# Kernel tuning notes

Measured on AMD Instinct MI355X. Metric: run time of the kernel, lower is better.

The kernel has to match this reference:

```python
import jax, jax.numpy as jnp
import numpy as np

D_STATE = 512
D_MODEL = 512
BATCH = 8
SEQ = 4096
DT_MIN, DT_MAX = 1e-3, 0.1
LN_EPS = 1e-5


def setup_inputs() -> dict:
    key = jax.random.key(0)
    ks = jax.random.split(key, 4)
    x = jax.random.normal(ks[0], (BATCH, SEQ, D_MODEL), dtype=jnp.float32)
    volatility_scale = jax.random.uniform(ks[1], (BATCH, SEQ, 1), dtype=jnp.float32)
    # parameters (mirroring the torch module's __init__)
    log_lambda_real = jnp.linspace(np.log(DT_MIN), np.log(DT_MAX), D_STATE).astype(jnp.float32)
    log_b = jax.random.uniform(ks[2], (D_STATE, 1), dtype=jnp.float32, minval=-0.5, maxval=0.5)
    c = jax.random.normal(ks[3], (1, D_STATE), dtype=jnp.float32) / np.sqrt(D_STATE)
    log_d = jnp.zeros((1,), jnp.float32)
    ts = np.array([1.0 / 24.0, 1.0, 5.0, 21.0, 63.0], np.float32)
    extra = np.linspace(63.0, 189.0, D_STATE - len(ts), dtype=np.float32)
    log_step = jnp.log(jnp.asarray(np.concatenate([ts, extra])))
    volatility_gate = jnp.ones((D_MODEL,), jnp.float32)
    alpha = jnp.asarray(0.7, jnp.float32)
    ln_weight = jnp.ones((D_STATE,), jnp.float32)
    ln_bias = jnp.zeros((D_STATE,), jnp.float32)
    return dict(x=x, volatility_scale=volatility_scale,
                log_lambda_real=log_lambda_real, log_b=log_b, c=c, log_d=log_d,
                log_step=log_step, volatility_gate=volatility_gate, alpha=alpha,
                ln_weight=ln_weight, ln_bias=ln_bias)


def reference(x, volatility_scale, log_lambda_real, log_b, c, log_d,
              log_step, volatility_gate, alpha, ln_weight, ln_bias):
    lam = -jnp.exp(log_lambda_real)              # [N], negative real poles
    step = jnp.exp(log_step)                     # [N], per-state timescale
    b = jnp.exp(log_b)[:, 0]                     # [N]
    d = jnp.exp(log_d)                           # [1], skip gain
    # bilinear (Tustin) discretization, paired per state
    z = step * lam                               # [N]
    a_disc = (2.0 + z) / (2.0 - z)               # [N]
    b_disc = step * (1.0 + a_disc) * b / 2.0     # [N]
    gate = jax.nn.sigmoid(volatility_gate)       # [D]
    c_vec = c[0]                                 # [N]

    def layer_norm(h):
        mu = jnp.mean(h, axis=-1, keepdims=True)
        var = jnp.var(h, axis=-1, keepdims=True)
        return (h - mu) * jax.lax.rsqrt(var + LN_EPS) * ln_weight + ln_bias

    def scan_step(h, inp):
        x_t, v_t = inp                           # [B,D], [B,1]
        h = a_disc * h + b_disc * x_t            # diagonal SSM update, [B,N]
        h = layer_norm(h)
        h = h / (1.0 + gate * v_t)               # volatility gating
        y_t = jnp.sum(h * c_vec, axis=-1, keepdims=True) + d * x_t  # [B,D]
        return h, y_t

    h0 = jnp.zeros((x.shape[0], a_disc.shape[0]), x.dtype)
    xs = (jnp.swapaxes(x, 0, 1), jnp.swapaxes(volatility_scale, 0, 1))  # time-major
    _, ys = jax.lax.scan(scan_step, h0, xs)      # [S,B,D]
    y = jnp.swapaxes(ys, 0, 1)                   # [B,S,D]
    al = jax.nn.sigmoid(alpha)
    return al * x + (1.0 - al) * y
```

## Files before the change

### kernel.cpp

```cpp
#include <hip/hip_runtime.h>
#include <cstdint>
#include <cstddef>

#define BATCH 8
#define SEQ   4096
#define DS    512
#define JPL   8
#define BLK   4
#define NB    (SEQ / BLK)

typedef float v2f __attribute__((ext_vector_type(2)));
typedef float v4f __attribute__((ext_vector_type(4)));

static __device__ __forceinline__ v2f lo2(v4f x) { return __builtin_shufflevector(x, x, 0, 1); }
static __device__ __forceinline__ v2f hi2(v4f x) { return __builtin_shufflevector(x, x, 2, 3); }

template <int CTRL>
__device__ __forceinline__ float dpp_add(float v) {
  int t = __builtin_amdgcn_update_dpp(0, __builtin_bit_cast(int, v), CTRL, 0xF, 0xF, true);
  return v + __builtin_bit_cast(float, t);
}
__device__ __forceinline__ float wave_sum64(float v) {
  v = dpp_add<0x111>(v);
  v = dpp_add<0x112>(v);
  v = dpp_add<0x114>(v);
  v = dpp_add<0x118>(v);
  v = dpp_add<0x142>(v);
  v = dpp_add<0x143>(v);
  return v;
}
__device__ __forceinline__ float bcast63(float v) {
  return __builtin_bit_cast(float, __builtin_amdgcn_readlane(__builtin_bit_cast(int, v), 63));
}

__global__ __launch_bounds__(256) void rg_kernel(const float* __restrict__ vol,
                                                 const float* __restrict__ vgat,
                                                 float* __restrict__ rg) {
  int idx = blockIdx.x * 256 + threadIdx.x;
  int nt  = idx & 127;
  int bt  = idx >> 7;
  float v = vol[bt];
  v4f g = *(const v4f*)(vgat + nt * 4);
  v4f r;
#pragma unroll
  for (int k = 0; k < 4; ++k) {
    float gg = 1.0f / (1.0f + expf(-g[k]));
    r[k] = 1.0f / (1.0f + gg * v);
  }
  *(v4f*)(rg + (size_t)idx * 4) = r;
}

template <bool RGP, bool PART>
__global__ __launch_bounds__(64, 1) void ssm_scan(
    const float* __restrict__ x, const float* __restrict__ vol,
    const float* __restrict__ llr, const float* __restrict__ logb,
    const float* __restrict__ cvec, const float* __restrict__ lstp,
    const float* __restrict__ vgat, const float* __restrict__ lnw,
    const float* __restrict__ lnb, const float* __restrict__ rg_g,
    float* __restrict__ outp)
{
  const int b    = blockIdx.x;
  const int lane = threadIdx.x;
  const int n0   = lane * JPL;

  v2f a[4], bd[4], w[4], bias[4], cc[4], gate[4];
#pragma unroll
  for (int j = 0; j < JPL; ++j) {
    int n = n0 + j;
    float lam = -expf(llr[n]);
    float st  = expf(lstp[n]);
    float z   = st * lam;
    float ad  = (2.0f + z) / (2.0f - z);
    a[j >> 1][j & 1]    = ad;
    bd[j >> 1][j & 1]   = st * (1.0f + ad) * expf(logb[n]) * 0.5f;
    w[j >> 1][j & 1]    = lnw[n];
    bias[j >> 1][j & 1] = lnb[n];
    cc[j >> 1][j & 1]   = cvec[n];
    gate[j >> 1][j & 1] = RGP ? 0.0f : (1.0f / (1.0f + expf(-vgat[n])));
  }

  const float* xp = x + (size_t)b * SEQ * DS + n0;
  const float* vp = vol + (size_t)b * SEQ;
  const float* rp = RGP ? (rg_g + (size_t)b * SEQ * DS + n0) : nullptr;
  float* pp = outp + (size_t)b * SEQ * (PART ? 64 : 1);

  v2f h[4];
#pragma unroll
  for (int k = 0; k < 4; ++k) h[k] = (v2f){0.0f, 0.0f};

  v4f XA[2 * BLK], XB[2 * BLK], RA[2 * BLK], RB[2 * BLK];
  v4f VA = {0, 0, 0, 0}, VB = {0, 0, 0, 0};

  auto load_blk = [&](v4f (&X)[2 * BLK], v4f (&R)[2 * BLK], v4f& V, int T) {
    const float* xb = xp + (size_t)T * DS;
#pragma unroll
    for (int u = 0; u < BLK; ++u) {
      X[2 * u]     = *(const v4f*)(xb + u * DS);
      X[2 * u + 1] = *(const v4f*)(xb + u * DS + 4);
    }
    if constexpr (RGP) {
      const float* rb = rp + (size_t)T * DS;
#pragma unroll
      for (int u = 0; u < BLK; ++u) {
        R[2 * u]     = *(const v4f*)(rb + u * DS);
        R[2 * u + 1] = *(const v4f*)(rb + u * DS + 4);
      }
    } else {
      V = *(const v4f*)(vp + T);
    }
  };

  auto proc_blk = [&](const v4f (&X)[2 * BLK], const v4f (&R)[2 * BLK], v4f V, int T) {
    float sacc[BLK];
#pragma unroll
    for (int u = 0; u < BLK; ++u) {
      v2f xs[4] = {lo2(X[2 * u]), hi2(X[2 * u]), lo2(X[2 * u + 1]), hi2(X[2 * u + 1])};

      v2f hr[4];
#pragma unroll
      for (int k = 0; k < 4; ++k)
        hr[k] = __builtin_elementwise_fma(a[k], h[k], bd[k] * xs[k]);

      v2f t01 = hr[0] + hr[1], t23 = hr[2] + hr[3];
      v2f ts = t01 + t23;
      float s1 = ts.x + ts.y;
      v2f q01 = hr[0] * hr[0] + hr[1] * hr[1];
      v2f q23 = hr[2] * hr[2] + hr[3] * hr[3];
      v2f qs = q01 + q23;
      float s2 = qs.x + qs.y;

      s1 = bcast63(wave_sum64(s1));
      s2 = bcast63(wave_sum64(s2));
      float mu  = s1 * (1.0f / DS);
      float m2  = s2 * (1.0f / DS);
      float var = __builtin_fmaf(-mu, mu, m2);
      float inv = __builtin_amdgcn_rsqf(var + 1e-5f);

      v2f rs[4];
      if constexpr (RGP) {
        rs[0] = lo2(R[2 * u]); rs[1] = hi2(R[2 * u]);
        rs[2] = lo2(R[2 * u + 1]); rs[3] = hi2(R[2 * u + 1]);
      } else {
        float vt = V[u];
#pragma unroll
        for (int k = 0; k < 4; ++k) {
          v2f den = gate[k] * vt + 1.0f;
          rs[k][0] = __builtin_amdgcn_rcpf(den[0]);
          rs[k][1] = __builtin_amdgcn_rcpf(den[1]);
        }
      }

#pragma unroll
      for (int k = 0; k < 4; ++k) {
        v2f niw = w[k] * inv;
        v2f hb  = bias[k] - niw * mu;
        v2f hln = __builtin_elementwise_fma(hr[k], niw, hb);
        h[k] = hln * rs[k];
      }

      v2f d = h[0] * cc[0];
      d = __builtin_elementwise_fma(h[1], cc[1], d);
      d = __builtin_elementwise_fma(h[2], cc[2], d);
      d = __builtin_elementwise_fma(h[3], cc[3], d);
      float sd = d.x + d.y;
      if constexpr (PART) sacc[u] = sd;
      else                sacc[u] = wave_sum64(sd);
    }
    if constexpr (PART) {
#pragma unroll
      for (int u = 0; u < BLK; ++u) pp[(size_t)(T + u) * 64 + lane] = sacc[u];
    } else {
      if (lane == 63) {
#pragma unroll
        for (int u = 0; u < BLK; ++u) pp[T + u] = sacc[u];
      }
    }
  };

  load_blk(XA, RA, VA, 0);
  __builtin_amdgcn_sched_barrier(0);
  int T = 0;
#pragma unroll 1
  for (int it = 0; it < NB / 2 - 1; ++it, T += 2 * BLK) {
    load_blk(XB, RB, VB, T + BLK);
    __builtin_amdgcn_sched_barrier(0);
    proc_blk(XA, RA, VA, T);
    __builtin_amdgcn_sched_barrier(0);
    load_blk(XA, RA, VA, T + 2 * BLK);
    __builtin_amdgcn_sched_barrier(0);
    proc_blk(XB, RB, VB, T + BLK);
    __builtin_amdgcn_sched_barrier(0);
  }
  load_blk(XB, RB, VB, T + BLK);
  proc_blk(XA, RA, VA, T);
  proc_blk(XB, RB, VB, T + BLK);
}

__global__ __launch_bounds__(256) void out_part(
    const float* __restrict__ x, const float* __restrict__ part,
    const float* __restrict__ alpha_p, const float* __restrict__ logd_p,
    float* __restrict__ out)
{
  const int lane = threadIdx.x & 63;
  const size_t bt = (size_t)blockIdx.x * 4 + (threadIdx.x >> 6);

  float al   = 1.0f / (1.0f + expf(-alpha_p[0]));
  float dd   = expf(logd_p[0]);
  float coef = __builtin_fmaf(1.0f - al, dd, al);
  float c1   = 1.0f - al;

  float p = part[bt * 64 + lane];
  float s = bcast63(wave_sum64(p)) * c1;

  const v4f* x4 = (const v4f*)x;
  v4f* o4 = (v4f*)out;
  size_t base = bt * 128;
#pragma unroll
  for (int j = 0; j < 2; ++j) {
    size_t i = base + lane + (size_t)j * 64;
    v4f xv = x4[i];
    o4[i] = xv * coef + s;
  }
}

__global__ __launch_bounds__(256) void out_scalar(
    const float* __restrict__ x, const float* __restrict__ sp,
    const float* __restrict__ alpha_p, const float* __restrict__ logd_p,
    float* __restrict__ out)
{
  const int lane = threadIdx.x & 63;
  const size_t bt = (size_t)blockIdx.x * 4 + (threadIdx.x >> 6);

  float al   = 1.0f / (1.0f + expf(-alpha_p[0]));
  float dd   = expf(logd_p[0]);
  float coef = __builtin_fmaf(1.0f - al, dd, al);
  float c1   = 1.0f - al;

  float s = sp[bt] * c1;
  const v4f* x4 = (const v4f*)x;
  v4f* o4 = (v4f*)out;
  size_t base = bt * 128;
#pragma unroll
  for (int j = 0; j < 2; ++j) {
    size_t i = base + lane + (size_t)j * 64;
    v4f xv = x4[i];
    o4[i] = xv * coef + s;
  }
}

extern "C" void kernel_launch(void* const* d_in, const int* in_sizes, int n_in,
                              void* d_out, int out_size, void* d_ws, size_t ws_size,
                              hipStream_t stream) {
  const float* x    = (const float*)d_in[0];
  const float* vol  = (const float*)d_in[1];
  const float* llr  = (const float*)d_in[2];
  const float* logb = (const float*)d_in[3];
  const float* cvec = (const float*)d_in[4];
  const float* logd = (const float*)d_in[5];
  const float* lstp = (const float*)d_in[6];
  const float* vgat = (const float*)d_in[7];
  const float* alph = (const float*)d_in[8];
  const float* lnw  = (const float*)d_in[9];
  const float* lnb  = (const float*)d_in[10];
  float* wsf = (float*)d_ws;
  float* outf = (float*)d_out;

  const size_t rg_elems   = (size_t)BATCH * SEQ * DS;
  const size_t part_elems = (size_t)BATCH * SEQ * 64;

  if (ws_size >= (rg_elems + part_elems) * sizeof(float)) {
    float* rg   = wsf;
    float* part = wsf + rg_elems;
    rg_kernel<<<(BATCH * SEQ * 128) / 256, 256, 0, stream>>>(vol, vgat, rg);
    ssm_scan<true, true><<<BATCH, 64, 0, stream>>>(x, vol, llr, logb, cvec, lstp,
                                                   vgat, lnw, lnb, rg, part);
    out_part<<<BATCH * SEQ / 4, 256, 0, stream>>>(x, part, alph, logd, outf);
  } else if (ws_size >= part_elems * sizeof(float)) {
    float* part = wsf;
    ssm_scan<false, true><<<BATCH, 64, 0, stream>>>(x, vol, llr, logb, cvec, lstp,
                                                    vgat, lnw, lnb, nullptr, part);
    out_part<<<BATCH * SEQ / 4, 256, 0, stream>>>(x, part, alph, logd, outf);
  } else {
    float* sp = wsf;
    ssm_scan<false, false><<<BATCH, 64, 0, stream>>>(x, vol, llr, logb, cvec, lstp,
                                                     vgat, lnw, lnb, nullptr, sp);
    out_scalar<<<BATCH * SEQ / 4, 256, 0, stream>>>(x, sp, alph, logd, outf);
  }
}
```

Before: 773.0 us.

## Warp-specialize scan with DMA producer, gating producer, and reduction consumer waves

Splits the per-batch scan block into three waves. One wave streams x into double-buffered LDS with global_load_lds and also finishes the output-projection reductions. A second wave computes the volatility-gating reciprocals into LDS. The third wave runs only the serial recurrence and LayerNorm. This removes the separate rg_kernel pass and its large workspace round-trip, takes the per-step cross-lane output reduction off the critical path, and doubles the block size to 8 steps. In exchange it adds two block-wide barriers per block and LDS traffic, with only 8 workgroups on the GPU.

```diff
diff --git a/kernel.cpp b/kernel.cpp
--- a/kernel.cpp
+++ b/kernel.cpp
@@ -6,8 +6,8 @@
 #define SEQ   4096
 #define DS    512
 #define JPL   8
-#define BLK   4
-#define NB    (SEQ / BLK)
+#define BLK   8
+#define NBLK  (SEQ / BLK)
 
 typedef float v2f __attribute__((ext_vector_type(2)));
 typedef float v4f __attribute__((ext_vector_type(4)));
@@ -33,193 +33,175 @@
   return __builtin_bit_cast(float, __builtin_amdgcn_readlane(__builtin_bit_cast(int, v), 63));
 }
 
-__global__ __launch_bounds__(256) void rg_kernel(const float* __restrict__ vol,
-                                                 const float* __restrict__ vgat,
-                                                 float* __restrict__ rg) {
-  int idx = blockIdx.x * 256 + threadIdx.x;
-  int nt  = idx & 127;
-  int bt  = idx >> 7;
-  float v = vol[bt];
-  v4f g = *(const v4f*)(vgat + nt * 4);
-  v4f r;
-#pragma unroll
-  for (int k = 0; k < 4; ++k) {
-    float gg = 1.0f / (1.0f + expf(-g[k]));
-    r[k] = 1.0f / (1.0f + gg * v);
-  }
-  *(v4f*)(rg + (size_t)idx * 4) = r;
-}
-
-template <bool RGP, bool PART>
-__global__ __launch_bounds__(64, 1) void ssm_scan(
+__device__ __forceinline__ void ld16(const float* g, float* l) {
+  __builtin_amdgcn_global_load_lds(
+      (const __attribute__((address_space(1))) void*)g,
+      (__attribute__((address_space(3))) void*)l, 16, 0, 0);
+}
+
+__global__ __launch_bounds__(192, 1) void ssm_scan(
     const float* __restrict__ x, const float* __restrict__ vol,
     const float* __restrict__ llr, const float* __restrict__ logb,
     const float* __restrict__ cvec, const float* __restrict__ lstp,
     const float* __restrict__ vgat, const float* __restrict__ lnw,
-    const float* __restrict__ lnb, const float* __restrict__ rg_g,
-    float* __restrict__ outp)
+    const float* __restrict__ lnb, float* __restrict__ sp)
 {
+  __shared__ float X0[4096], X1[4096];
+  __shared__ float R0[4096], R1[4096];
+  __shared__ float SC0[512], SC1[512];
+
   const int b    = blockIdx.x;
-  const int lane = threadIdx.x;
-  const int n0   = lane * JPL;
-
-  v2f a[4], bd[4], w[4], bias[4], cc[4], gate[4];
-#pragma unroll
-  for (int j = 0; j < JPL; ++j) {
-    int n = n0 + j;
-    float lam = -expf(llr[n]);
-    float st  = expf(lstp[n]);
-    float z   = st * lam;
-    float ad  = (2.0f + z) / (2.0f - z);
-    a[j >> 1][j & 1]    = ad;
-    bd[j >> 1][j & 1]   = st * (1.0f + ad) * expf(logb[n]) * 0.5f;
-    w[j >> 1][j & 1]    = lnw[n];
-    bias[j >> 1][j & 1] = lnb[n];
-    cc[j >> 1][j & 1]   = cvec[n];
-    gate[j >> 1][j & 1] = RGP ? 0.0f : (1.0f / (1.0f + expf(-vgat[n])));
-  }
-
-  const float* xp = x + (size_t)b * SEQ * DS + n0;
-  const float* vp = vol + (size_t)b * SEQ;
-  const float* rp = RGP ? (rg_g + (size_t)b * SEQ * DS + n0) : nullptr;
-  float* pp = outp + (size_t)b * SEQ * (PART ? 64 : 1);
-
-  v2f h[4];
-#pragma unroll
-  for (int k = 0; k < 4; ++k) h[k] = (v2f){0.0f, 0.0f};
-
-  v4f XA[2 * BLK], XB[2 * BLK], RA[2 * BLK], RB[2 * BLK];
-  v4f VA = {0, 0, 0, 0}, VB = {0, 0, 0, 0};
-
-  auto load_blk = [&](v4f (&X)[2 * BLK], v4f (&R)[2 * BLK], v4f& V, int T) {
-    const float* xb = xp + (size_t)T * DS;
-#pragma unroll
-    for (int u = 0; u < BLK; ++u) {
-      X[2 * u]     = *(const v4f*)(xb + u * DS);
-      X[2 * u + 1] = *(const v4f*)(xb + u * DS + 4);
-    }
-    if constexpr (RGP) {
-      const float* rb = rp + (size_t)T * DS;
+  const int lane = threadIdx.x & 63;
+  const int wid  = threadIdx.x >> 6;
+
+  if (wid == 1) {
+    const float* xg = x + (size_t)b * SEQ * DS + lane * JPL;
+    float* spb = sp + (size_t)b * SEQ;
+
+    auto dma_blk = [&](int blk, float* Xs) {
 #pragma unroll
       for (int u = 0; u < BLK; ++u) {
-        R[2 * u]     = *(const v4f*)(rb + u * DS);
-        R[2 * u + 1] = *(const v4f*)(rb + u * DS + 4);
-      }
-    } else {
-      V = *(const v4f*)(vp + T);
-    }
-  };
-
-  auto proc_blk = [&](const v4f (&X)[2 * BLK], const v4f (&R)[2 * BLK], v4f V, int T) {
-    float sacc[BLK];
-#pragma unroll
-    for (int u = 0; u < BLK; ++u) {
-      v2f xs[4] = {lo2(X[2 * u]), hi2(X[2 * u]), lo2(X[2 * u + 1]), hi2(X[2 * u + 1])};
-
-      v2f hr[4];
-#pragma unroll
-      for (int k = 0; k < 4; ++k)
-        hr[k] = __builtin_elementwise_fma(a[k], h[k], bd[k] * xs[k]);
-
-      v2f t01 = hr[0] + hr[1], t23 = hr[2] + hr[3];
-      v2f ts = t01 + t23;
-      float s1 = ts.x + ts.y;
-      v2f q01 = hr[0] * hr[0] + hr[1] * hr[1];
-      v2f q23 = hr[2] * hr[2] + hr[3] * hr[3];
-      v2f qs = q01 + q23;
-      float s2 = qs.x + qs.y;
-
-      s1 = bcast63(wave_sum64(s1));
-      s2 = bcast63(wave_sum64(s2));
-      float mu  = s1 * (1.0f / DS);
-      float m2  = s2 * (1.0f / DS);
-      float var = __builtin_fmaf(-mu, mu, m2);
-      float inv = __builtin_amdgcn_rsqf(var + 1e-5f);
-
-      v2f rs[4];
-      if constexpr (RGP) {
-        rs[0] = lo2(R[2 * u]); rs[1] = hi2(R[2 * u]);
-        rs[2] = lo2(R[2 * u + 1]); rs[3] = hi2(R[2 * u + 1]);
-      } else {
-        float vt = V[u];
+        const float* row = xg + (size_t)(blk * BLK + u) * DS;
+        ld16(row,     Xs + u * 512);
+        ld16(row + 4, Xs + u * 512 + 256);
+      }
+    };
+    auto red_copy = [&](const float* SCs, int blk) {
+      float s[BLK];
+#pragma unroll
+      for (int u = 0; u < BLK; ++u) s[u] = wave_sum64(SCs[u * 64 + lane]);
+      if (lane == 63) {
+#pragma unroll
+        for (int u = 0; u < BLK; ++u) spb[blk * BLK + u] = s[u];
+      }
+    };
+
+    dma_blk(0, X0);
+    __syncthreads();
+#pragma unroll 1
+    for (int i2 = 0; i2 < NBLK; i2 += 2) {
+      dma_blk(i2 + 1, X1);
+      if (i2 > 0) red_copy(SC1, i2 - 1);
+      __syncthreads();
+      if (i2 + 2 < NBLK) dma_blk(i2 + 2, X0);
+      red_copy(SC0, i2);
+      __syncthreads();
+    }
+    red_copy(SC1, NBLK - 1);
+  } else if (wid == 2) {
+    v2f gate[4];
+#pragma unroll
+    for (int j = 0; j < JPL; ++j)
+      gate[j >> 1][j & 1] = 1.0f / (1.0f + expf(-vgat[lane * JPL + j]));
+    const float* vg = vol + (size_t)b * SEQ;
+
+    auto rg_blk = [&](v4f Va, v4f Vb, float* Rs) {
+#pragma unroll
+      for (int u = 0; u < BLK; ++u) {
+        float vt = (u < 4) ? Va[u] : Vb[u - 4];
+        v4f r0, r1;
 #pragma unroll
         for (int k = 0; k < 4; ++k) {
           v2f den = gate[k] * vt + 1.0f;
-          rs[k][0] = __builtin_amdgcn_rcpf(den[0]);
-          rs[k][1] = __builtin_amdgcn_rcpf(den[1]);
+          float q0 = __builtin_amdgcn_rcpf(den.x);
+          float q1 = __builtin_amdgcn_rcpf(den.y);
+          if (k < 2) { r0[2 * k] = q0; r0[2 * k + 1] = q1; }
+          else       { r1[2 * (k - 2)] = q0; r1[2 * (k - 2) + 1] = q1; }
         }
-      }
-
-#pragma unroll
-      for (int k = 0; k < 4; ++k) {
-        v2f niw = w[k] * inv;
-        v2f hb  = bias[k] - niw * mu;
-        v2f hln = __builtin_elementwise_fma(hr[k], niw, hb);
-        h[k] = hln * rs[k];
-      }
-
-      v2f d = h[0] * cc[0];
-      d = __builtin_elementwise_fma(h[1], cc[1], d);
-      d = __builtin_elementwise_fma(h[2], cc[2], d);
-      d = __builtin_elementwise_fma(h[3], cc[3], d);
-      float sd = d.x + d.y;
-      if constexpr (PART) sacc[u] = sd;
-      else                sacc[u] = wave_sum64(sd);
-    }
-    if constexpr (PART) {
-#pragma unroll
-      for (int u = 0; u < BLK; ++u) pp[(size_t)(T + u) * 64 + lane] = sacc[u];
-    } else {
-      if (lane == 63) {
-#pragma unroll
-        for (int u = 0; u < BLK; ++u) pp[T + u] = sacc[u];
-      }
-    }
-  };
-
-  load_blk(XA, RA, VA, 0);
-  __builtin_amdgcn_sched_barrier(0);
-  int T = 0;
+        *(v4f*)(Rs + u * 512 + lane * 4)       = r0;
+        *(v4f*)(Rs + u * 512 + 256 + lane * 4) = r1;
+      }
+    };
+
+    v4f V0a = *(const v4f*)(vg + 0), V0b = *(const v4f*)(vg + 4);
+    v4f V1a = *(const v4f*)(vg + 8), V1b = *(const v4f*)(vg + 12);
+    rg_blk(V0a, V0b, R0);
+    __syncthreads();
 #pragma unroll 1
-  for (int it = 0; it < NB / 2 - 1; ++it, T += 2 * BLK) {
-    load_blk(XB, RB, VB, T + BLK);
-    __builtin_amdgcn_sched_barrier(0);
-    proc_blk(XA, RA, VA, T);
-    __builtin_amdgcn_sched_barrier(0);
-    load_blk(XA, RA, VA, T + 2 * BLK);
-    __builtin_amdgcn_sched_barrier(0);
-    proc_blk(XB, RB, VB, T + BLK);
-    __builtin_amdgcn_sched_barrier(0);
-  }
-  load_blk(XB, RB, VB, T + BLK);
-  proc_blk(XA, RA, VA, T);
-  proc_blk(XB, RB, VB, T + BLK);
-}
-
-__global__ __launch_bounds__(256) void out_part(
-    const float* __restrict__ x, const float* __restrict__ part,
-    const float* __restrict__ alpha_p, const float* __restrict__ logd_p,
-    float* __restrict__ out)
-{
-  const int lane = threadIdx.x & 63;
-  const size_t bt = (size_t)blockIdx.x * 4 + (threadIdx.x >> 6);
-
-  float al   = 1.0f / (1.0f + expf(-alpha_p[0]));
-  float dd   = expf(logd_p[0]);
-  float coef = __builtin_fmaf(1.0f - al, dd, al);
-  float c1   = 1.0f - al;
-
-  float p = part[bt * 64 + lane];
-  float s = bcast63(wave_sum64(p)) * c1;
-
-  const v4f* x4 = (const v4f*)x;
-  v4f* o4 = (v4f*)out;
-  size_t base = bt * 128;
-#pragma unroll
-  for (int j = 0; j < 2; ++j) {
-    size_t i = base + lane + (size_t)j * 64;
-    v4f xv = x4[i];
-    o4[i] = xv * coef + s;
+    for (int i2 = 0; i2 < NBLK; i2 += 2) {
+      if (i2 + 2 < NBLK) {
+        V0a = *(const v4f*)(vg + (i2 + 2) * BLK);
+        V0b = *(const v4f*)(vg + (i2 + 2) * BLK + 4);
+      }
+      rg_blk(V1a, V1b, R1);
+      __syncthreads();
+      if (i2 + 3 < NBLK) {
+        V1a = *(const v4f*)(vg + (i2 + 3) * BLK);
+        V1b = *(const v4f*)(vg + (i2 + 3) * BLK + 4);
+      }
+      if (i2 + 2 < NBLK) rg_blk(V0a, V0b, R0);
+      __syncthreads();
+    }
+  } else {
+    v2f a[4], bd[4], w[4], bias[4], cc[4];
+#pragma unroll
+    for (int j = 0; j < JPL; ++j) {
+      int n = lane * JPL + j;
+      float lam = -expf(llr[n]);
+      float st  = expf(lstp[n]);
+      float z   = st * lam;
+      float ad  = (2.0f + z) / (2.0f - z);
+      a[j >> 1][j & 1]    = ad;
+      bd[j >> 1][j & 1]   = st * (1.0f + ad) * expf(logb[n]) * 0.5f;
+      w[j >> 1][j & 1]    = lnw[n];
+      bias[j >> 1][j & 1] = lnb[n];
+      cc[j >> 1][j & 1]   = cvec[n];
+    }
+    v2f h[4];
+#pragma unroll
+    for (int k = 0; k < 4; ++k) h[k] = (v2f){0.0f, 0.0f};
+
+    auto proc_blk = [&](const float* Xs, const float* Rs, float* SCs) {
+#pragma unroll
+      for (int u = 0; u < BLK; ++u) {
+        v4f xx0 = *(const v4f*)(Xs + u * 512 + lane * 4);
+        v4f xx1 = *(const v4f*)(Xs + u * 512 + 256 + lane * 4);
+        v4f rr0 = *(const v4f*)(Rs + u * 512 + lane * 4);
+        v4f rr1 = *(const v4f*)(Rs + u * 512 + 256 + lane * 4);
+        v2f xs[4] = {lo2(xx0), hi2(xx0), lo2(xx1), hi2(xx1)};
+        v2f rs[4] = {lo2(rr0), hi2(rr0), lo2(rr1), hi2(rr1)};
+
+        v2f hr[4];
+#pragma unroll
+        for (int k = 0; k < 4; ++k)
+          hr[k] = __builtin_elementwise_fma(a[k], h[k], bd[k] * xs[k]);
+
+        v2f ts = (hr[0] + hr[1]) + (hr[2] + hr[3]);
+        float s1 = ts.x + ts.y;
+        v2f qs = (hr[0] * hr[0] + hr[1] * hr[1]) + (hr[2] * hr[2] + hr[3] * hr[3]);
+        float s2 = qs.x + qs.y;
+
+        s1 = bcast63(wave_sum64(s1));
+        s2 = bcast63(wave_sum64(s2));
+        float mu  = s1 * (1.0f / DS);
+        float m2  = s2 * (1.0f / DS);
+        float var = __builtin_fmaf(-mu, mu, m2);
+        float inv = __builtin_amdgcn_rsqf(var + 1e-5f);
+
+#pragma unroll
+        for (int k = 0; k < 4; ++k) {
+          v2f niw = w[k] * inv;
+          v2f hb  = bias[k] - niw * mu;
+          v2f hln = __builtin_elementwise_fma(hr[k], niw, hb);
+          h[k] = hln * rs[k];
+        }
+
+        v2f d = h[0] * cc[0];
+        d = __builtin_elementwise_fma(h[1], cc[1], d);
+        d = __builtin_elementwise_fma(h[2], cc[2], d);
+        d = __builtin_elementwise_fma(h[3], cc[3], d);
+        SCs[u * 64 + lane] = d.x + d.y;
+      }
+    };
+
+    __syncthreads();
+#pragma unroll 1
+    for (int i2 = 0; i2 < NBLK; i2 += 2) {
+      proc_blk(X0, R0, SC0);
+      __syncthreads();
+      proc_blk(X1, R1, SC1);
+      __syncthreads();
+    }
   }
 }
 
@@ -262,28 +244,10 @@
   const float* alph = (const float*)d_in[8];
   const float* lnw  = (const float*)d_in[9];
   const float* lnb  = (const float*)d_in[10];
-  float* wsf = (float*)d_ws;
+  float* sp   = (float*)d_ws;
   float* outf = (float*)d_out;
 
-  const size_t rg_elems   = (size_t)BATCH * SEQ * DS;
-  const size_t part_elems = (size_t)BATCH * SEQ * 64;
-
-  if (ws_size >= (rg_elems + part_elems) * sizeof(float)) {
-    float* rg   = wsf;
-    float* part = wsf + rg_elems;
-    rg_kernel<<<(BATCH * SEQ * 128) / 256, 256, 0, stream>>>(vol, vgat, rg);
-    ssm_scan<true, true><<<BATCH, 64, 0, stream>>>(x, vol, llr, logb, cvec, lstp,
-                                                   vgat, lnw, lnb, rg, part);
-    out_part<<<BATCH * SEQ / 4, 256, 0, stream>>>(x, part, alph, logd, outf);
-  } else if (ws_size >= part_elems * sizeof(float)) {
-    float* part = wsf;
-    ssm_scan<false, true><<<BATCH, 64, 0, stream>>>(x, vol, llr, logb, cvec, lstp,
-                                                    vgat, lnw, lnb, nullptr, part);
-    out_part<<<BATCH * SEQ / 4, 256, 0, stream>>>(x, part, alph, logd, outf);
-  } else {
-    float* sp = wsf;
-    ssm_scan<false, false><<<BATCH, 64, 0, stream>>>(x, vol, llr, logb, cvec, lstp,
-                                                     vgat, lnw, lnb, nullptr, sp);
-    out_scalar<<<BATCH * SEQ / 4, 256, 0, stream>>>(x, sp, alph, logd, outf);
-  }
-}
+  ssm_scan<<<BATCH, 192, 0, stream>>>(x, vol, llr, logb, cvec, lstp,
+                                      vgat, lnw, lnb, sp);
+  out_scalar<<<BATCH * SEQ / 4, 256, 0, stream>>>(x, sp, alph, logd, outf);
+}
```

Measured after the change: 697.2 us. 1.11x faster.
